# Kernel optimization log

Measured on AMD Instinct MI355X. Metric: run time of the kernel, lower is better.

## Reference

```python
import jax, jax.numpy as jnp
import numpy as np

BOX = 100.0      # points live in [0, BOX)^3
STRIDE = 128     # > BOX/voxel_size, used for linearizing 3D voxel coords


def setup_inputs() -> dict:
    key = jax.random.key(0)
    k1, k2 = jax.random.split(key)
    N, C = 2_000_000, 32
    positions = jax.random.uniform(k1, (N, 3), dtype=jnp.float32) * BOX
    features = jax.random.normal(k2, (N, C), dtype=jnp.float32)
    voxel_size = jnp.ones((), dtype=jnp.float32)
    return {"positions": positions, "features": features, "voxel_size": voxel_size}


def reference(positions, features, voxel_size):
    """VoxelPooling(position_fn='center', feature_fn='max').

    Output is padded to N rows (M <= N real voxels); `valid` marks real voxels.
    Voxel grid is aligned to the origin; pooled position is the voxel center.
    """
    N = positions.shape[0]
    # integer voxel coordinates (positions are non-negative here)
    coords = jnp.floor(positions / voxel_size).astype(jnp.int32)           # [N,3]
    lin = coords[:, 0] + STRIDE * coords[:, 1] + STRIDE * STRIDE * coords[:, 2]  # [N]
    # compact unique voxels; jit-compatible with fixed size=N, pad with -1
    uniq, inv = jnp.unique(lin, size=N, fill_value=-1, return_inverse=True)
    # per-voxel max over features (empty segments get dtype-min, masked below)
    pooled_features = jax.ops.segment_max(features, inv, num_segments=N)   # [N,C]
    # decode voxel coords from linear key -> voxel centers
    cz = uniq // (STRIDE * STRIDE)
    rem = uniq % (STRIDE * STRIDE)
    cy = rem // STRIDE
    cx = rem % STRIDE
    centers = (jnp.stack([cx, cy, cz], axis=-1).astype(positions.dtype) + 0.5) * voxel_size
    valid = uniq >= 0                                                      # [N]
    pooled_positions = jnp.where(valid[:, None], centers, 0.0)
    pooled_features = jnp.where(valid[:, None], pooled_features, 0.0)
    return pooled_positions, pooled_features, valid
```

## Files before the change

### kernel.cpp

```cpp
#include <hip/hip_runtime.h>
#include <stdint.h>

#define STRIDE 128
#define NVOX (STRIDE * STRIDE * STRIDE)
#define BINVOX 512
#define NBIN (NVOX / BINVOX)
#define HB 256
#define HT 1024
#define NSEG 16
#define SEGBINS (NBIN / NSEG)

typedef unsigned long long u64;

__device__ __forceinline__ uint32_t enc_f32(float f) {
  uint32_t u = __float_as_uint(f);
  return (u & 0x80000000u) ? ~u : (u | 0x80000000u);
}
__device__ __forceinline__ float dec_f32(uint32_t e) {
  uint32_t u = (e & 0x80000000u) ? (e & 0x7fffffffu) : ~e;
  return __uint_as_float(u);
}

__device__ __forceinline__ uint32_t cnt_eq1(uint32_t w) {
  uint32_t y = w ^ 0x01010101u;
  uint32_t z = ~(((y & 0x7F7F7F7Fu) + 0x7F7F7F7Fu) | y | 0x7F7F7F7Fu);
  return __popc(z);
}

__global__ __launch_bounds__(HT) void k_hist(const float* __restrict__ pos,
                                             const float* __restrict__ vs_p,
                                             int* __restrict__ lin_arr,
                                             uint8_t* __restrict__ bytemap,
                                             uint32_t* __restrict__ hist,
                                             uint32_t* __restrict__ sync, int n) {
  __shared__ uint32_t h[NBIN];
  int b = blockIdx.x, t = threadIdx.x;
  if (b == 0 && t == 0) *sync = 0u;
  for (int k = t; k < NBIN; k += HT) h[k] = 0u;
  __syncthreads();
  int chunk = (n + HB - 1) / HB;
  int i0 = b * chunk, i1 = min(n, i0 + chunk);
  float vs = vs_p[0];
  for (int i = i0 + t; i < i1; i += HT) {
    float x = pos[3 * (size_t)i + 0];
    float y = pos[3 * (size_t)i + 1];
    float z = pos[3 * (size_t)i + 2];
    int lin = (int)floorf(x / vs) + STRIDE * (int)floorf(y / vs) +
              STRIDE * STRIDE * (int)floorf(z / vs);
    lin_arr[i] = lin;
    bytemap[lin] = 1;
    atomicAdd(&h[lin >> 9], 1u);
  }
  __syncthreads();
  for (int k = t; k < NBIN; k += HT) hist[(size_t)b * NBIN + k] = h[k];
}

__global__ __launch_bounds__(SEGBINS) void k_scan(
    const uint32_t* __restrict__ hist, const uint32_t* __restrict__ bytemap_w,
    uint32_t* __restrict__ base2, u64* __restrict__ tot2,
    uint32_t* __restrict__ bin_base, uint32_t* __restrict__ occ_base,
    uint32_t* __restrict__ sync, u64* __restrict__ seg_tot,
    uint32_t* __restrict__ Mp) {
  __shared__ u64 s[SEGBINS];
  int b = blockIdx.x, t = threadIdx.x;
  int bin = b * SEGBINS + t;
  uint32_t run = 0;
  #pragma unroll 8
  for (int c = 0; c < HB; ++c) {
    base2[(size_t)c * NBIN + bin] = run;
    run += hist[(size_t)c * NBIN + bin];
  }
  const uint4* bp = (const uint4*)bytemap_w + (size_t)bin * 32;
  uint32_t occ = 0;
  #pragma unroll
  for (int k = 0; k < 32; ++k) {
    uint4 v = bp[k];
    occ += cnt_eq1(v.x) + cnt_eq1(v.y) + cnt_eq1(v.z) + cnt_eq1(v.w);
  }
  u64 mine = (u64)run | ((u64)occ << 32);
  tot2[bin] = mine;
  s[t] = mine;
  __syncthreads();
  for (int off = 1; off < SEGBINS; off <<= 1) {
    u64 a = (t >= off) ? s[t - off] : 0ull;
    __syncthreads();
    s[t] += a;
    __syncthreads();
  }
  u64 excl = s[t] - mine;
  u64 blk_total = s[SEGBINS - 1];
  if (t == 0) {
    __hip_atomic_store(&seg_tot[b], blk_total, __ATOMIC_RELEASE,
                       __HIP_MEMORY_SCOPE_AGENT);
    __hip_atomic_fetch_add(sync, 1u, __ATOMIC_ACQ_REL, __HIP_MEMORY_SCOPE_AGENT);
    while (__hip_atomic_load(sync, __ATOMIC_ACQUIRE, __HIP_MEMORY_SCOPE_AGENT) <
           (uint32_t)NSEG) {}
  }
  __syncthreads();
  u64 pre = 0, grand = 0;
  #pragma unroll
  for (int i = 0; i < NSEG; ++i) {
    u64 v = __hip_atomic_load(&seg_tot[i], __ATOMIC_ACQUIRE,
                              __HIP_MEMORY_SCOPE_AGENT);
    if (i < b) pre += v;
    grand += v;
  }
  u64 g = pre + excl;
  bin_base[bin] = (uint32_t)g;
  occ_base[bin] = (uint32_t)(g >> 32);
  if (b == 0 && t == 0) Mp[0] = (uint32_t)(grand >> 32);
}

__global__ __launch_bounds__(HT) void k_part(const int* __restrict__ lin_arr,
                                             const uint32_t* __restrict__ bin_base,
                                             const uint32_t* __restrict__ base2,
                                             uint32_t* __restrict__ pairs, int n) {
  __shared__ uint32_t cur[NBIN];
  int b = blockIdx.x, t = threadIdx.x;
  for (int k = t; k < NBIN; k += HT)
    cur[k] = bin_base[k] + base2[(size_t)b * NBIN + k];
  __syncthreads();
  int chunk = (n + HB - 1) / HB;
  int i0 = b * chunk, i1 = min(n, i0 + chunk);
  for (int i = i0 + t; i < i1; i += HT) {
    int lin = lin_arr[i];
    uint32_t slot = atomicAdd(&cur[lin >> 9], 1u);
    pairs[slot] = ((uint32_t)(lin & (BINVOX - 1)) << 21) | (uint32_t)i;
  }
}

__global__ __launch_bounds__(1024) void k_pool(
    const float* __restrict__ feat, const float* __restrict__ vs_p,
    const uint32_t* __restrict__ pairs, const uint32_t* __restrict__ bin_base,
    const u64* __restrict__ tot2, const uint32_t* __restrict__ occ_base,
    const uint8_t* __restrict__ bytemap, const uint32_t* __restrict__ Mp,
    float* __restrict__ out_pos, float* __restrict__ out_feat,
    float* __restrict__ out_valid, int n, int srow) {
  __shared__ uint32_t smax[BINVOX * 32];
  __shared__ u64 sbw[8];
  int t = threadIdx.x;

  if (blockIdx.x >= NBIN) {
    size_t gid = (size_t)(blockIdx.x - NBIN) * 1024 + t;
    int row = (int)(gid >> 3);
    int q = (int)(gid & 7);
    if (row >= n) return;
    uint32_t M = Mp[0];
    if ((uint32_t)row < M) return;
    if (row < srow)
      ((float4*)out_feat)[(size_t)row * 8 + q] = make_float4(0.f, 0.f, 0.f, 0.f);
    if (q == 0) {
      out_pos[(size_t)row * 3 + 0] = 0.f;
      out_pos[(size_t)row * 3 + 1] = 0.f;
      out_pos[(size_t)row * 3 + 2] = 0.f;
      out_valid[row] = 0.f;
    }
    return;
  }

  int bin = blockIdx.x;
  uint32_t cnt = (uint32_t)tot2[bin];
  if (cnt == 0) return;
  uint32_t start = bin_base[bin];

  #pragma unroll
  for (int k = 0; k < 16; ++k) smax[t + k * 1024] = 0u;
  if (t < 512) {
    uint32_t occb = bytemap[(size_t)bin * BINVOX + t];
    u64 m = __ballot(occb == 1u);
    if ((t & 63) == 0) sbw[t >> 6] = m;
  }
  __syncthreads();

  int g = t >> 5;
  int ch = t & 31;
  uint32_t last = cnt - 1;
  for (uint32_t u = (uint32_t)g; u < cnt; u += 256) {
    uint32_t p0 = pairs[start + u];
    uint32_t p1 = pairs[start + min(u + 32u, last)];
    uint32_t p2 = pairs[start + min(u + 64u, last)];
    uint32_t p3 = pairs[start + min(u + 96u, last)];
    uint32_t p4 = pairs[start + min(u + 128u, last)];
    uint32_t p5 = pairs[start + min(u + 160u, last)];
    uint32_t p6 = pairs[start + min(u + 192u, last)];
    uint32_t p7 = pairs[start + min(u + 224u, last)];
    float v0 = feat[(size_t)(p0 & 0x1FFFFFu) * 32 + ch];
    float v1 = feat[(size_t)(p1 & 0x1FFFFFu) * 32 + ch];
    float v2 = feat[(size_t)(p2 & 0x1FFFFFu) * 32 + ch];
    float v3 = feat[(size_t)(p3 & 0x1FFFFFu) * 32 + ch];
    float v4 = feat[(size_t)(p4 & 0x1FFFFFu) * 32 + ch];
    float v5 = feat[(size_t)(p5 & 0x1FFFFFu) * 32 + ch];
    float v6 = feat[(size_t)(p6 & 0x1FFFFFu) * 32 + ch];
    float v7 = feat[(size_t)(p7 & 0x1FFFFFu) * 32 + ch];
    atomicMax(&smax[(p0 >> 21) * 32 + ch], enc_f32(v0));
    atomicMax(&smax[(p1 >> 21) * 32 + ch], enc_f32(v1));
    atomicMax(&smax[(p2 >> 21) * 32 + ch], enc_f32(v2));
    atomicMax(&smax[(p3 >> 21) * 32 + ch], enc_f32(v3));
    atomicMax(&smax[(p4 >> 21) * 32 + ch], enc_f32(v4));
    atomicMax(&smax[(p5 >> 21) * 32 + ch], enc_f32(v5));
    atomicMax(&smax[(p6 >> 21) * 32 + ch], enc_f32(v6));
    atomicMax(&smax[(p7 >> 21) * 32 + ch], enc_f32(v7));
  }
  __syncthreads();

  int vb = t >> 1, half = t & 1;
  u64 w = sbw[vb >> 6];
  int bit = vb & 63;
  if ((w >> bit) & 1ull) {
    uint32_t lr = (uint32_t)__popcll(w & ((1ull << bit) - 1ull));
    for (int ww = 0; ww < (vb >> 6); ++ww) lr += (uint32_t)__popcll(sbw[ww]);
    uint32_t rank = occ_base[bin] + lr;
    float4* orow = (float4*)(out_feat + (size_t)rank * 32 + half * 16);
    #pragma unroll
    for (int j = 0; j < 4; ++j) {
      const uint32_t* sp = &smax[vb * 32 + half * 16 + j * 4];
      float4 o;
      o.x = dec_f32(sp[0]); o.y = dec_f32(sp[1]);
      o.z = dec_f32(sp[2]); o.w = dec_f32(sp[3]);
      orow[j] = o;
    }
    if (half == 0) {
      float vs = vs_p[0];
      int lin = bin * BINVOX + vb;
      int cx = lin & 127, cy = (lin >> 7) & 127, cz = lin >> 14;
      out_pos[(size_t)rank * 3 + 0] = ((float)cx + 0.5f) * vs;
      out_pos[(size_t)rank * 3 + 1] = ((float)cy + 0.5f) * vs;
      out_pos[(size_t)rank * 3 + 2] = ((float)cz + 0.5f) * vs;
      out_valid[rank] = 1.0f;
    }
  }
}

__global__ void k_tail2(float4* __restrict__ dst, long long cnt4) {
  long long i = (long long)blockIdx.x * blockDim.x + threadIdx.x;
  if (i < cnt4) dst[i] = make_float4(0.f, 0.f, 0.f, 0.f);
}

extern "C" void kernel_launch(void* const* d_in, const int* in_sizes, int n_in,
                              void* d_out, int out_size, void* d_ws, size_t ws_size,
                              hipStream_t stream) {
  const float* pos  = (const float*)d_in[0];
  const float* feat = (const float*)d_in[1];
  const float* vs   = (const float*)d_in[2];
  int n = in_sizes[0] / 3;

  float*    out_pos   = (float*)d_out;
  uint32_t* out_feat  = (uint32_t*)(out_pos + (size_t)n * 3);
  float*    out_valid = (float*)((float*)out_feat + (size_t)n * 32);

  size_t scratch_u32 = 2 * (size_t)n + 2 * (size_t)HB * NBIN +
                       2 * (size_t)NBIN + 2 * (size_t)NBIN + NVOX / 4;
  uint32_t* scratch  = out_feat + (size_t)n * 32 - scratch_u32;
  int*      lin      = (int*)scratch;
  uint32_t* pairs    = scratch + n;
  uint32_t* hist     = pairs + n;
  uint32_t* base2    = hist + (size_t)HB * NBIN;
  u64*      tot2     = (u64*)(base2 + (size_t)HB * NBIN);
  uint32_t* bin_base = (uint32_t*)(tot2 + NBIN);
  uint32_t* occ_base = bin_base + NBIN;
  uint8_t*  bytemap  = (uint8_t*)(occ_base + NBIN);

  int srow = (int)(((size_t)n * 32 - scratch_u32) / 32);

  uint32_t* Mp   = (uint32_t*)d_ws;
  uint32_t* sync = Mp + 1;
  u64*      seg_tot = (u64*)(Mp + 2);

  k_hist<<<HB, HT, 0, stream>>>(pos, vs, lin, bytemap, hist, sync, n);
  k_scan<<<NSEG, SEGBINS, 0, stream>>>(hist, (const uint32_t*)bytemap, base2,
                                       tot2, bin_base, occ_base, sync, seg_tot, Mp);
  k_part<<<HB, HT, 0, stream>>>(lin, bin_base, base2, pairs, n);
  int tail_blocks = (int)(((size_t)n * 8 + 1023) / 1024);
  k_pool<<<NBIN + tail_blocks, 1024, 0, stream>>>(
      feat, vs, pairs, bin_base, tot2, occ_base, bytemap, Mp,
      out_pos, (float*)out_feat, out_valid, n, srow);
  long long cnt4 = ((long long)n * 32 - (long long)srow * 32) / 4;
  k_tail2<<<(int)((cnt4 + 1023) / 1024), 1024, 0, stream>>>(
      (float4*)(out_feat + (size_t)srow * 32), cnt4);
}
```

Before: 222.7 us.

## Replace global cross-block histogram scan with per-block local offsets and binary-search lookup

Each histogram block now does a local exclusive scan over its own bins and writes block-local offsets. This removes the serial 256-step column scan in k_scan, which previously wrote base2 and read hist. k_part partitions each block's points into its own contiguous chunk, and k_pool rebuilds a bin's element list by scanning per-block counts and binary-searching to map logical indices to pair slots. Scratch memory moves into the workspace when it is large enough, which lets the tail-zeroing kernel be skipped. The cost is eight extra shared-memory binary searches per gathered element in k_pool, plus a small scan at the start of every bin block.

```diff
diff --git a/kernel.cpp b/kernel.cpp
--- a/kernel.cpp
+++ b/kernel.cpp
@@ -27,13 +27,28 @@
   return __popc(z);
 }
 
+__device__ __forceinline__ uint32_t src_of(uint32_t u, const uint32_t* csum,
+                                           const uint32_t* offs) {
+  uint32_t lo = 0, hi = HB - 1;
+  #pragma unroll
+  for (int it = 0; it < 8; ++it) {
+    uint32_t mid = (lo + hi) >> 1;
+    bool gt = csum[mid] > u;
+    hi = gt ? mid : hi;
+    lo = gt ? lo : mid + 1;
+  }
+  uint32_t prev = lo ? csum[lo - 1] : 0u;
+  return offs[lo] + (u - prev);
+}
+
 __global__ __launch_bounds__(HT) void k_hist(const float* __restrict__ pos,
                                              const float* __restrict__ vs_p,
                                              int* __restrict__ lin_arr,
                                              uint8_t* __restrict__ bytemap,
-                                             uint32_t* __restrict__ hist,
+                                             uint32_t* __restrict__ loff,
                                              uint32_t* __restrict__ sync, int n) {
   __shared__ uint32_t h[NBIN];
+  __shared__ uint32_t s[HT];
   int b = blockIdx.x, t = threadIdx.x;
   if (b == 0 && t == 0) *sync = 0u;
   for (int k = t; k < NBIN; k += HT) h[k] = 0u;
@@ -52,24 +67,31 @@
     atomicAdd(&h[lin >> 9], 1u);
   }
   __syncthreads();
-  for (int k = t; k < NBIN; k += HT) hist[(size_t)b * NBIN + k] = h[k];
+  uint32_t v0 = h[t * 4 + 0], v1 = h[t * 4 + 1], v2 = h[t * 4 + 2], v3 = h[t * 4 + 3];
+  uint32_t sum = v0 + v1 + v2 + v3;
+  s[t] = sum;
+  __syncthreads();
+  for (int off = 1; off < HT; off <<= 1) {
+    uint32_t a = (t >= off) ? s[t - off] : 0u;
+    __syncthreads();
+    s[t] += a;
+    __syncthreads();
+  }
+  uint32_t run = s[t] - sum;
+  uint32_t* lr = &loff[(size_t)b * NBIN + t * 4];
+  lr[0] = run; run += v0;
+  lr[1] = run; run += v1;
+  lr[2] = run; run += v2;
+  lr[3] = run;
 }
 
 __global__ __launch_bounds__(SEGBINS) void k_scan(
-    const uint32_t* __restrict__ hist, const uint32_t* __restrict__ bytemap_w,
-    uint32_t* __restrict__ base2, u64* __restrict__ tot2,
-    uint32_t* __restrict__ bin_base, uint32_t* __restrict__ occ_base,
-    uint32_t* __restrict__ sync, u64* __restrict__ seg_tot,
+    const uint32_t* __restrict__ bytemap_w, uint32_t* __restrict__ occ_base,
+    uint32_t* __restrict__ sync, uint32_t* __restrict__ seg_tot,
     uint32_t* __restrict__ Mp) {
-  __shared__ u64 s[SEGBINS];
+  __shared__ uint32_t s[SEGBINS];
   int b = blockIdx.x, t = threadIdx.x;
   int bin = b * SEGBINS + t;
-  uint32_t run = 0;
-  #pragma unroll 8
-  for (int c = 0; c < HB; ++c) {
-    base2[(size_t)c * NBIN + bin] = run;
-    run += hist[(size_t)c * NBIN + bin];
-  }
   const uint4* bp = (const uint4*)bytemap_w + (size_t)bin * 32;
   uint32_t occ = 0;
   #pragma unroll
@@ -77,51 +99,45 @@
     uint4 v = bp[k];
     occ += cnt_eq1(v.x) + cnt_eq1(v.y) + cnt_eq1(v.z) + cnt_eq1(v.w);
   }
-  u64 mine = (u64)run | ((u64)occ << 32);
-  tot2[bin] = mine;
-  s[t] = mine;
+  s[t] = occ;
   __syncthreads();
   for (int off = 1; off < SEGBINS; off <<= 1) {
-    u64 a = (t >= off) ? s[t - off] : 0ull;
+    uint32_t a = (t >= off) ? s[t - off] : 0u;
     __syncthreads();
     s[t] += a;
     __syncthreads();
   }
-  u64 excl = s[t] - mine;
-  u64 blk_total = s[SEGBINS - 1];
+  uint32_t excl = s[t] - occ;
   if (t == 0) {
-    __hip_atomic_store(&seg_tot[b], blk_total, __ATOMIC_RELEASE,
+    __hip_atomic_store(&seg_tot[b], s[SEGBINS - 1], __ATOMIC_RELEASE,
                        __HIP_MEMORY_SCOPE_AGENT);
     __hip_atomic_fetch_add(sync, 1u, __ATOMIC_ACQ_REL, __HIP_MEMORY_SCOPE_AGENT);
     while (__hip_atomic_load(sync, __ATOMIC_ACQUIRE, __HIP_MEMORY_SCOPE_AGENT) <
            (uint32_t)NSEG) {}
   }
   __syncthreads();
-  u64 pre = 0, grand = 0;
+  uint32_t pre = 0, grand = 0;
   #pragma unroll
   for (int i = 0; i < NSEG; ++i) {
-    u64 v = __hip_atomic_load(&seg_tot[i], __ATOMIC_ACQUIRE,
-                              __HIP_MEMORY_SCOPE_AGENT);
+    uint32_t v = __hip_atomic_load(&seg_tot[i], __ATOMIC_ACQUIRE,
+                                   __HIP_MEMORY_SCOPE_AGENT);
     if (i < b) pre += v;
     grand += v;
   }
-  u64 g = pre + excl;
-  bin_base[bin] = (uint32_t)g;
-  occ_base[bin] = (uint32_t)(g >> 32);
-  if (b == 0 && t == 0) Mp[0] = (uint32_t)(grand >> 32);
+  occ_base[bin] = pre + excl;
+  if (b == 0 && t == 0) Mp[0] = grand;
 }
 
 __global__ __launch_bounds__(HT) void k_part(const int* __restrict__ lin_arr,
-                                             const uint32_t* __restrict__ bin_base,
-                                             const uint32_t* __restrict__ base2,
+                                             const uint32_t* __restrict__ loff,
                                              uint32_t* __restrict__ pairs, int n) {
   __shared__ uint32_t cur[NBIN];
   int b = blockIdx.x, t = threadIdx.x;
-  for (int k = t; k < NBIN; k += HT)
-    cur[k] = bin_base[k] + base2[(size_t)b * NBIN + k];
-  __syncthreads();
   int chunk = (n + HB - 1) / HB;
   int i0 = b * chunk, i1 = min(n, i0 + chunk);
+  for (int k = t; k < NBIN; k += HT)
+    cur[k] = (uint32_t)i0 + loff[(size_t)b * NBIN + k];
+  __syncthreads();
   for (int i = i0 + t; i < i1; i += HT) {
     int lin = lin_arr[i];
     uint32_t slot = atomicAdd(&cur[lin >> 9], 1u);
@@ -131,13 +147,14 @@
 
 __global__ __launch_bounds__(1024) void k_pool(
     const float* __restrict__ feat, const float* __restrict__ vs_p,
-    const uint32_t* __restrict__ pairs, const uint32_t* __restrict__ bin_base,
-    const u64* __restrict__ tot2, const uint32_t* __restrict__ occ_base,
-    const uint8_t* __restrict__ bytemap, const uint32_t* __restrict__ Mp,
+    const uint32_t* __restrict__ pairs, const uint32_t* __restrict__ loff,
+    const uint32_t* __restrict__ occ_base, const uint8_t* __restrict__ bytemap,
+    const uint32_t* __restrict__ Mp,
     float* __restrict__ out_pos, float* __restrict__ out_feat,
     float* __restrict__ out_valid, int n, int srow) {
   __shared__ uint32_t smax[BINVOX * 32];
   __shared__ u64 sbw[8];
+  __shared__ uint32_t offs[HB], csum[HB];
   int t = threadIdx.x;
 
   if (blockIdx.x >= NBIN) {
@@ -159,10 +176,6 @@
   }
 
   int bin = blockIdx.x;
-  uint32_t cnt = (uint32_t)tot2[bin];
-  if (cnt == 0) return;
-  uint32_t start = bin_base[bin];
-
   #pragma unroll
   for (int k = 0; k < 16; ++k) smax[t + k * 1024] = 0u;
   if (t < 512) {
@@ -170,20 +183,40 @@
     u64 m = __ballot(occb == 1u);
     if ((t & 63) == 0) sbw[t >> 6] = m;
   }
-  __syncthreads();
+  int chunk = (n + HB - 1) / HB;
+  if (t < HB) {
+    int b = t;
+    int i0b = b * chunk, i1b = min(n, i0b + chunk);
+    uint32_t lo = loff[(size_t)b * NBIN + bin];
+    uint32_t hi = (bin == NBIN - 1) ? (uint32_t)(i1b - i0b)
+                                    : loff[(size_t)b * NBIN + bin + 1];
+    offs[t] = (uint32_t)i0b + lo;
+    csum[t] = hi - lo;
+  }
+  __syncthreads();
+  for (int off = 1; off < HB; off <<= 1) {
+    uint32_t a = (t >= off && t < HB) ? csum[t - off] : 0u;
+    __syncthreads();
+    if (t < HB) csum[t] += a;
+    __syncthreads();
+  }
+  uint32_t cnt = csum[HB - 1];
+  if (cnt == 0) return;
 
   int g = t >> 5;
   int ch = t & 31;
   uint32_t last = cnt - 1;
   for (uint32_t u = (uint32_t)g; u < cnt; u += 256) {
-    uint32_t p0 = pairs[start + u];
-    uint32_t p1 = pairs[start + min(u + 32u, last)];
-    uint32_t p2 = pairs[start + min(u + 64u, last)];
-    uint32_t p3 = pairs[start + min(u + 96u, last)];
-    uint32_t p4 = pairs[start + min(u + 128u, last)];
-    uint32_t p5 = pairs[start + min(u + 160u, last)];
-    uint32_t p6 = pairs[start + min(u + 192u, last)];
-    uint32_t p7 = pairs[start + min(u + 224u, last)];
+    uint32_t s0 = src_of(u, csum, offs);
+    uint32_t s1 = src_of(min(u + 32u, last), csum, offs);
+    uint32_t s2 = src_of(min(u + 64u, last), csum, offs);
+    uint32_t s3 = src_of(min(u + 96u, last), csum, offs);
+    uint32_t s4 = src_of(min(u + 128u, last), csum, offs);
+    uint32_t s5 = src_of(min(u + 160u, last), csum, offs);
+    uint32_t s6 = src_of(min(u + 192u, last), csum, offs);
+    uint32_t s7 = src_of(min(u + 224u, last), csum, offs);
+    uint32_t p0 = pairs[s0], p1 = pairs[s1], p2 = pairs[s2], p3 = pairs[s3];
+    uint32_t p4 = pairs[s4], p5 = pairs[s5], p6 = pairs[s6], p7 = pairs[s7];
     float v0 = feat[(size_t)(p0 & 0x1FFFFFu) * 32 + ch];
     float v1 = feat[(size_t)(p1 & 0x1FFFFFu) * 32 + ch];
     float v2 = feat[(size_t)(p2 & 0x1FFFFFu) * 32 + ch];
@@ -248,33 +281,39 @@
   uint32_t* out_feat  = (uint32_t*)(out_pos + (size_t)n * 3);
   float*    out_valid = (float*)((float*)out_feat + (size_t)n * 32);
 
-  size_t scratch_u32 = 2 * (size_t)n + 2 * (size_t)HB * NBIN +
-                       2 * (size_t)NBIN + 2 * (size_t)NBIN + NVOX / 4;
-  uint32_t* scratch  = out_feat + (size_t)n * 32 - scratch_u32;
-  int*      lin      = (int*)scratch;
-  uint32_t* pairs    = scratch + n;
-  uint32_t* hist     = pairs + n;
-  uint32_t* base2    = hist + (size_t)HB * NBIN;
-  u64*      tot2     = (u64*)(base2 + (size_t)HB * NBIN);
-  uint32_t* bin_base = (uint32_t*)(tot2 + NBIN);
-  uint32_t* occ_base = bin_base + NBIN;
+  size_t scratch_u32 = 2 * (size_t)n + (size_t)HB * NBIN + NBIN + NVOX / 4;
+  size_t ws_need = 256 + scratch_u32 * 4;
+
+  uint32_t* Mp      = (uint32_t*)d_ws;
+  uint32_t* sync    = Mp + 1;
+  uint32_t* seg_tot = Mp + 8;
+
+  uint32_t* base;
+  int srow;
+  if (ws_size >= ws_need) {
+    base = (uint32_t*)((char*)d_ws + 256);
+    srow = n;
+  } else {
+    base = out_feat + (size_t)n * 32 - scratch_u32;
+    srow = (int)(((size_t)n * 32 - scratch_u32) / 32);
+  }
+  int*      lin      = (int*)base;
+  uint32_t* pairs    = base + n;
+  uint32_t* loff     = pairs + n;
+  uint32_t* occ_base = loff + (size_t)HB * NBIN;
   uint8_t*  bytemap  = (uint8_t*)(occ_base + NBIN);
 
-  int srow = (int)(((size_t)n * 32 - scratch_u32) / 32);
-
-  uint32_t* Mp   = (uint32_t*)d_ws;
-  uint32_t* sync = Mp + 1;
-  u64*      seg_tot = (u64*)(Mp + 2);
-
-  k_hist<<<HB, HT, 0, stream>>>(pos, vs, lin, bytemap, hist, sync, n);
-  k_scan<<<NSEG, SEGBINS, 0, stream>>>(hist, (const uint32_t*)bytemap, base2,
-                                       tot2, bin_base, occ_base, sync, seg_tot, Mp);
-  k_part<<<HB, HT, 0, stream>>>(lin, bin_base, base2, pairs, n);
+  k_hist<<<HB, HT, 0, stream>>>(pos, vs, lin, bytemap, loff, sync, n);
+  k_scan<<<NSEG, SEGBINS, 0, stream>>>((const uint32_t*)bytemap, occ_base, sync,
+                                       seg_tot, Mp);
+  k_part<<<HB, HT, 0, stream>>>(lin, loff, pairs, n);
   int tail_blocks = (int)(((size_t)n * 8 + 1023) / 1024);
   k_pool<<<NBIN + tail_blocks, 1024, 0, stream>>>(
-      feat, vs, pairs, bin_base, tot2, occ_base, bytemap, Mp,
+      feat, vs, pairs, loff, occ_base, bytemap, Mp,
       out_pos, (float*)out_feat, out_valid, n, srow);
-  long long cnt4 = ((long long)n * 32 - (long long)srow * 32) / 4;
-  k_tail2<<<(int)((cnt4 + 1023) / 1024), 1024, 0, stream>>>(
-      (float4*)(out_feat + (size_t)srow * 32), cnt4);
-}
+  if (srow < n) {
+    long long cnt4 = ((long long)n * 32 - (long long)srow * 32) / 4;
+    k_tail2<<<(int)((cnt4 + 1023) / 1024), 1024, 0, stream>>>(
+        (float4*)(out_feat + (size_t)srow * 32), cnt4);
+  }
+}
```

After: 274.4 us. 23.2% more time.
